# Kernel tuning notes

Measured on AMD Instinct MI355X. Metric: run time of the kernel, lower is better.

Reference implementation:

```python
import jax, jax.numpy as jnp
import numpy as np

EPS = 1e-5
SELECT_NUM = 10   # hard-coded in Support_AUG_Image
NEIGHBOR_K = 3
SEMI_K = 3


def _conv(x, w):
    return jax.lax.conv_general_dilated(x, w, (1, 1), 'SAME',
                                        dimension_numbers=('NCHW', 'OIHW', 'NCHW'))


def _bn(x, g, b):
    # BatchNorm2d, training mode: biased batch stats over (N, H, W)
    mu = jnp.mean(x, (0, 2, 3), keepdims=True)
    var = jnp.mean((x - mu) ** 2, (0, 2, 3), keepdims=True)
    return g[None, :, None, None] * (x - mu) * jax.lax.rsqrt(var + EPS) + b[None, :, None, None]


def _lrelu(x):
    return jnp.where(x >= 0, x, 0.2 * x)


def _pool(x):
    return jax.lax.reduce_window(x, -jnp.inf, jax.lax.max,
                                 (1, 1, 2, 2), (1, 1, 2, 2), 'VALID')


def _features(x, params):
    # conv-bn-lrelu-pool, conv-bn-lrelu-pool, conv-bn-lrelu, conv-bn-lrelu
    for i, (w, g, b) in enumerate(params):
        x = _lrelu(_bn(_conv(x, w), g, b))
        if i < 2:
            x = _pool(x)
    return x  # [N, 64, 21, 21] for 84x84 input


def _descriptors(feat):
    # [B, C, h, w] -> [B, h*w, C], rows L2-normalized (query local descriptors)
    B, C = feat.shape[0], feat.shape[1]
    d = feat.reshape(B, C, -1).transpose(0, 2, 1)
    return d / jnp.sqrt(jnp.sum(d * d, -1, keepdims=True))


def _col_normalize(s):
    # [C, m]: L2-normalize each column (support descriptor)
    return s / jnp.sqrt(jnp.sum(s * s, 0, keepdims=True))


def _img2class_sim(q_desc, S, k):
    # q_desc [B, n, C] row-normalized; S [K, C, m] raw support banks.
    # Per class (K small, fixed): cosine sims [B, n, m], top-k over m, sum.
    sims = []
    for j in range(S.shape[0]):
        inner = q_desc @ _col_normalize(S[j])          # [B, n, m]
        tv = jax.lax.top_k(inner, k)[0]                # [B, n, k]
        sims.append(jnp.sum(tv, axis=(1, 2)))
    return jnp.stack(sims, 1)                          # [B, K]


def _forward(input1, input2, input3, params):
    K, shot = input2.shape[0], input2.shape[1]
    q = _features(input1, params)                      # [Bq, 64, 21, 21]
    sup = _features(input2.reshape((-1,) + input2.shape[2:]), params)
    C, h, w = sup.shape[1], sup.shape[2], sup.shape[3]
    # per class: permute(1,0,2,3).view(C,-1) -> [K, C, shot*h*w]
    S = sup.reshape(K, shot, C, h, w).transpose(0, 2, 1, 3, 4).reshape(K, C, shot * h * w)
    u = _features(input3, params)                      # [Bu, 64, 21, 21]

    # Support_AUG_Image: similarity of unlabeled pool vs support, softmax over classes,
    # then append top-10 unlabeled feature maps (raw) to each class bank.
    u_desc = _descriptors(u)
    sim_u = jax.nn.softmax(_img2class_sim(u_desc, S, SEMI_K), axis=1)  # [Bu, K]
    aug = []
    for j in range(K):
        idx = jax.lax.top_k(sim_u[:, j], SELECT_NUM)[1]                # [10]
        sel = u[idx].transpose(1, 0, 2, 3).reshape(C, -1)              # [C, 10*h*w]
        aug.append(jnp.concatenate([S[j], sel], axis=1))
    S_aug = jnp.stack(aug, 0)                          # [K, C, shot*h*w + 10*h*w]

    # ImgtoClass_Metric on queries vs augmented support
    q_desc = _descriptors(q)
    return _img2class_sim(q_desc, S_aug, NEIGHBOR_K)   # [Bq, K]


def setup_inputs() -> dict:
    key = jax.random.key(0)
    ks = jax.random.split(key, 8)
    inp = {
        'input1': jax.random.normal(ks[0], (75, 3, 84, 84), jnp.float32),
        'input2': jax.random.normal(ks[1], (5, 5, 3, 84, 84), jnp.float32),
        'input3': jax.random.normal(ks[2], (64, 3, 84, 84), jnp.float32),
        'w1': jax.random.normal(ks[3], (64, 3, 3, 3), jnp.float32) * 0.1,
        'w2': jax.random.normal(ks[4], (64, 64, 3, 3), jnp.float32) * 0.05,
        'w3': jax.random.normal(ks[5], (64, 64, 3, 3), jnp.float32) * 0.05,
        'w4': jax.random.normal(ks[6], (64, 64, 3, 3), jnp.float32) * 0.05,
    }
    for i in (1, 2, 3, 4):
        inp[f'g{i}'] = jnp.ones((64,), jnp.float32)
        inp[f'b{i}'] = jnp.zeros((64,), jnp.float32)
    return inp


def reference(input1, input2, input3, w1, g1, b1, w2, g2, b2, w3, g3, b3, w4, g4, b4):
    params = [(w1, g1, b1), (w2, g2, b2), (w3, g3, b3), (w4, g4, b4)]
    return _forward(input1, input2, input3, params)
```

## Files before the change

kernel.cpp:

```cpp
#include <hip/hip_runtime.h>
#include <hip/hip_bf16.h>
#include <math.h>

typedef __hip_bfloat16 bf16;
typedef __attribute__((ext_vector_type(8))) short short8;
typedef __attribute__((ext_vector_type(4))) float floatx4;
typedef __attribute__((ext_vector_type(4))) unsigned short ushort4v;

#define LRELU(v) ((v) < 0.f ? 0.2f * (v) : (v))

__device__ __forceinline__ float b2f(bf16 x) { return __bfloat162float(x); }
__device__ __forceinline__ int img_group(int n) { return n < 75 ? 0 : (n < 100 ? 1 : 2); }

__global__ __launch_bounds__(64) void detect_kernel(
    const void* in1, const void* in2, const void* in3,
    const void* w1, const void* w2, const void* w3, const void* w4,
    const void* g1, const void* g2, const void* g3, const void* g4,
    int* __restrict__ flags)
{
  int t = threadIdx.x;
  if (t >= 11) return;
  const void* p = nullptr; int nh = 384, isg = 0;
  switch (t) {
    case 0: p = in1; break;  case 1: p = in2; break;  case 2: p = in3; break;
    case 3: p = w1;  break;  case 4: p = w2;  break;  case 5: p = w3;  break;
    case 6: p = w4;  break;
    case 7: p = g1; nh = 64; isg = 1; break;
    case 8: p = g2; nh = 64; isg = 1; break;
    case 9: p = g3; nh = 64; isg = 1; break;
    case 10: p = g4; nh = 64; isg = 1; break;
  }
  const unsigned short* h = (const unsigned short*)p;
  int cnt = 0;
  for (int i = 0; i < nh; ++i) {
    unsigned short v = h[i];
    if (isg) {
      if (v == 0) ++cnt;
    } else {
      int e = (v >> 7) & 0xFF;
      if (e >= 160 || (e > 0 && e <= 80)) ++cnt;
    }
  }
  flags[t] = isg ? (cnt >= 16) : (cnt >= 48);
}

#define NIMG 3471552
#define BIMG 13562
#define NWP  110592
#define BWP  432
#define BW1  8
#define BGB  2
#define NPART (4 * 164 * 128)
#define NZ (NPART + 320 + 375)
#define BZ  331
__global__ __launch_bounds__(256) void setup_all(
    const void* in1, const void* in2, const void* in3,
    const void* w1, const void* w2, const void* w3, const void* w4,
    const void* g1, const void* b1, const void* g2, const void* b2,
    const void* g3, const void* b3, const void* g4, const void* b4,
    const int* __restrict__ flags,
    bf16* __restrict__ imgp, bf16* __restrict__ w1p,
    bf16* __restrict__ wp2, bf16* __restrict__ wp3, bf16* __restrict__ wp4,
    float* __restrict__ gb, float* __restrict__ part,
    float* __restrict__ uscore, float* __restrict__ qscore)
{
  int b = blockIdx.x;
  if (b < BIMG) {
    int k = b * 256 + threadIdx.x;
    if (k >= NIMG) return;
    const void* src; int idx, f;
    if (k < 75 * 21168)       { src = in1; idx = k;               f = flags[0]; }
    else if (k < 100 * 21168) { src = in2; idx = k - 75 * 21168;  f = flags[1]; }
    else                      { src = in3; idx = k - 100 * 21168; f = flags[2]; }
    bf16 v = f ? __float2bfloat16(((const float*)src)[idx]) : ((const bf16*)src)[idx];
    int n = k / 21168, r = k % 21168;
    int ci = r / 7056, pix = r % 7056;
    int y = pix / 84, x = pix % 84;
    imgp[((size_t)(n * 3 + ci) * 86 + y + 1) * 86 + x + 1] = v;
  } else if (b < BIMG + BWP) {
    int idx = (b - BIMG) * 256 + threadIdx.x;
    if (idx >= NWP) return;
    int which = idx / 36864, i = idx % 36864;
    const void* src = which == 0 ? w2 : (which == 1 ? w3 : w4);
    bf16* dst = which == 0 ? wp2 : (which == 1 ? wp3 : wp4);
    int f = flags[4 + which];
    float v = f ? ((const float*)src)[i] : b2f(((const bf16*)src)[i]);
    int co = i / 576, ci = (i / 9) % 64, tap = i % 9;
    dst[((size_t)tap * 64 + co) * 64 + ci] = __float2bfloat16(v);
  } else if (b < BIMG + BWP + BW1) {
    int i = (b - BIMG - BWP) * 256 + threadIdx.x;
    if (i >= 2048) return;
    int co = i >> 5, k = i & 31;
    float v = 0.f;
    if (k < 27) {
      int f = flags[3];
      v = f ? ((const float*)w1)[co * 27 + k] : b2f(((const bf16*)w1)[co * 27 + k]);
    }
    w1p[i] = __float2bfloat16(v);
  } else if (b < BIMG + BWP + BW1 + BGB) {
    int i = (b - BIMG - BWP - BW1) * 256 + threadIdx.x;
    if (i >= 512) return;
    int which = i >> 6, cc = i & 63;
    const void* s;
    switch (which) {
      case 0: s = g1; break; case 1: s = b1; break;
      case 2: s = g2; break; case 3: s = b2; break;
      case 4: s = g3; break; case 5: s = b3; break;
      case 6: s = g4; break; default: s = b4; break;
    }
    int isg = !(which & 1);
    int f = isg ? flags[7 + (which >> 1)] : 0;
    gb[i] = f ? ((const float*)s)[cc] : b2f(((const bf16*)s)[cc]);
  } else {
    int i = (b - BIMG - BWP - BW1 - BGB) * 256 + threadIdx.x;
    if (i < NPART) part[i] = 0.f;
    else if (i < NPART + 320) uscore[i - NPART] = 0.f;
    else if (i < NZ) qscore[i - NPART - 320] = 0.f;
  }
}

__global__ __launch_bounds__(256) void conv1_stats_mfma(
    const bf16* __restrict__ imgp, const bf16* __restrict__ w1p,
    float* __restrict__ part)
{
  __shared__ float sacc[128];
  int n = blockIdx.x, tile = blockIdx.y;
  int lane = threadIdx.x & 63;
  int q = lane >> 4, c = lane & 15;
  int wave = threadIdx.x >> 6;
  int p = tile * 64 + wave * 16 + c;
  bool valid = p < 7056;
  int pc = valid ? p : 0;
  int y = pc / 84, x = pc % 84;
  const short* ib = (const short*)(imgp + (size_t)n * 3 * 86 * 86);
  short bs[8];
  #pragma unroll
  for (int j = 0; j < 8; ++j) {
    int k = q * 8 + j;
    int ci = k / 9, tap = k - ci * 9;
    int dy = tap / 3, dx = tap - dy * 3;
    bs[j] = (k < 27 && valid) ? ib[(ci * 86 + y + dy) * 86 + x + dx] : (short)0;
  }
  short8 B = {bs[0], bs[1], bs[2], bs[3], bs[4], bs[5], bs[6], bs[7]};
  float s[16], sq[16];
  #pragma unroll
  for (int t = 0; t < 4; ++t) {
    const short* ap = (const short*)w1p + (t * 16 + c) * 32 + q * 8;
    short8 A = *(const short8*)ap;
    floatx4 acc = {0.f, 0.f, 0.f, 0.f};
    acc = __builtin_amdgcn_mfma_f32_16x16x32_bf16(A, B, acc, 0, 0, 0);
    #pragma unroll
    for (int r = 0; r < 4; ++r) { s[t * 4 + r] = acc[r]; sq[t * 4 + r] = acc[r] * acc[r]; }
  }
  #pragma unroll
  for (int off = 1; off < 16; off <<= 1)
    #pragma unroll
    for (int i = 0; i < 16; ++i) {
      s[i]  += __shfl_xor(s[i], off);
      sq[i] += __shfl_xor(sq[i], off);
    }
  if (threadIdx.x < 128) sacc[threadIdx.x] = 0.f;
  __syncthreads();
  if (c == 0) {
    #pragma unroll
    for (int t = 0; t < 4; ++t)
      #pragma unroll
      for (int r = 0; r < 4; ++r) {
        int co = t * 16 + q * 4 + r;
        atomicAdd(&sacc[co], s[t * 4 + r]);
        atomicAdd(&sacc[64 + co], sq[t * 4 + r]);
      }
  }
  __syncthreads();
  if (threadIdx.x < 128) atomicAdd(&part[n * 128 + threadIdx.x], sacc[threadIdx.x]);
}

__global__ __launch_bounds__(256) void finalize_kernel(
    const float* __restrict__ part, const float* __restrict__ gam, const float* __restrict__ bet,
    float* __restrict__ scl, float* __restrict__ sht, float HWf)
{
  int t = threadIdx.x;
  if (t >= 192) return;
  int g = t / 64, c = t % 64;
  const int starts[3] = {0, 75, 100}, cnts[3] = {75, 25, 64};
  float S = 0.f, Q = 0.f;
  for (int im = starts[g]; im < starts[g] + cnts[g]; ++im) {
    S += part[im * 128 + c];
    Q += part[im * 128 + 64 + c];
  }
  float N = (float)cnts[g] * HWf;
  float mean = S / N;
  float var = fmaxf(Q / N - mean * mean, 0.f);
  float rstd = rsqrtf(var + 1e-5f);
  float sc = gam[c] * rstd;
  scl[t] = sc;
  sht[t] = bet[c] - mean * sc;
}

__global__ __launch_bounds__(256) void conv1_pool_mfma(
    const bf16* __restrict__ imgp, const bf16* __restrict__ w1p,
    const float* __restrict__ scl, const float* __restrict__ sht,
    bf16* __restrict__ p1t)
{
  int n = blockIdx.x, tile = blockIdx.y;
  int lane = threadIdx.x & 63, wave = threadIdx.x >> 6;
  int q = lane >> 4, c = lane & 15;
  int pp = tile * 64 + wave * 16 + c;
  bool valid = pp < 1764;
  int pc = valid ? pp : 0;
  int py = pc / 42, px = pc % 42;
  int g = img_group(n);
  const short* ib = (const short*)(imgp + (size_t)n * 3 * 86 * 86);
  short8 B[4];
  #pragma unroll
  for (int quad = 0; quad < 4; ++quad) {
    int y = 2 * py + (quad >> 1), x = 2 * px + (quad & 1);
    short bs[8];
    #pragma unroll
    for (int j = 0; j < 8; ++j) {
      int k = q * 8 + j;
      int ci = k / 9, tap = k - ci * 9;
      int dy = tap / 3, dx = tap - dy * 3;
      bs[j] = (k < 27) ? ib[(ci * 86 + y + dy) * 86 + x + dx] : (short)0;
    }
    B[quad] = (short8){bs[0], bs[1], bs[2], bs[3], bs[4], bs[5], bs[6], bs[7]};
  }
  bf16* ob = p1t + ((size_t)n * 1936 + (py + 1) * 44 + px + 1) * 64;
  #pragma unroll
  for (int t = 0; t < 4; ++t) {
    const short* ap = (const short*)w1p + (t * 16 + c) * 32 + q * 8;
    short8 A = *(const short8*)ap;
    floatx4 a0 = {0.f,0.f,0.f,0.f}, a1 = a0, a2 = a0, a3 = a0;
    a0 = __builtin_amdgcn_mfma_f32_16x16x32_bf16(A, B[0], a0, 0, 0, 0);
    a1 = __builtin_amdgcn_mfma_f32_16x16x32_bf16(A, B[1], a1, 0, 0, 0);
    a2 = __builtin_amdgcn_mfma_f32_16x16x32_bf16(A, B[2], a2, 0, 0, 0);
    a3 = __builtin_amdgcn_mfma_f32_16x16x32_bf16(A, B[3], a3, 0, 0, 0);
    if (valid) {
      ushort4v st;
      #pragma unroll
      for (int r = 0; r < 4; ++r) {
        int co = t * 16 + q * 4 + r;
        float sc_ = scl[g * 64 + co], sh_ = sht[g * 64 + co];
        float v0 = a0[r] * sc_ + sh_; v0 = LRELU(v0);
        float v1 = a1[r] * sc_ + sh_; v1 = LRELU(v1);
        float v2 = a2[r] * sc_ + sh_; v2 = LRELU(v2);
        float v3 = a3[r] * sc_ + sh_; v3 = LRELU(v3);
        float best = fmaxf(fmaxf(v0, v1), fmaxf(v2, v3));
        bf16 bv = __float2bfloat16(best);
        st[r] = *(unsigned short*)&bv;
      }
      *(ushort4v*)(ob + t * 16 + q * 4) = st;
    }
  }
}

__global__ __launch_bounds__(256) void tpad_kernel(
    const bf16* __restrict__ in, bf16* __restrict__ outp,
    int HW, int W, int PW, int PHPW)
{
  __shared__ bf16 tile[64][65];
  int n = blockIdx.x, t0 = blockIdx.y * 64;
  for (int idx = threadIdx.x; idx < 4096; idx += 256) {
    int ci = idx >> 6, pix = idx & 63;
    int p = t0 + pix;
    tile[pix][ci] = (p < HW) ? in[((size_t)n * 64 + ci) * HW + p] : __float2bfloat16(0.f);
  }
  __syncthreads();
  for (int idx = threadIdx.x; idx < 4096; idx += 256) {
    int pix = idx >> 6, ci = idx & 63;
    int p = t0 + pix;
    if (p < HW) {
      int y = p / W, x = p % W;
      outp[((size_t)n * PHPW + (y + 1) * PW + (x + 1)) * 64 + ci] = tile[pix][ci];
    }
  }
}

__global__ __launch_bounds__(256) void bnt_kernel(
    const float* __restrict__ in, const float* __restrict__ scl, const float* __restrict__ sht,
    bf16* __restrict__ outp, int HW, int W, int PW, int PHPW)
{
  __shared__ bf16 tile[64][65];
  int n = blockIdx.x, t0 = blockIdx.y * 64;
  int g = img_group(n);
  for (int idx = threadIdx.x; idx < 4096; idx += 256) {
    int ci = idx >> 6, pix = idx & 63;
    int p = t0 + pix;
    float v = 0.f;
    if (p < HW) {
      v = in[((size_t)n * 64 + ci) * HW + p] * scl[g * 64 + ci] + sht[g * 64 + ci];
      v = LRELU(v);
    }
    tile[pix][ci] = __float2bfloat16(v);
  }
  __syncthreads();
  for (int idx = threadIdx.x; idx < 4096; idx += 256) {
    int pix = idx >> 6, ci = idx & 63;
    int p = t0 + pix;
    if (p < HW) {
      int y = p / W, x = p % W;
      outp[((size_t)n * PHPW + (y + 1) * PW + (x + 1)) * 64 + ci] = tile[pix][ci];
    }
  }
}

__global__ __launch_bounds__(256) void conv_mfma_kernel(
    const bf16* __restrict__ in_t, const bf16* __restrict__ wp,
    void* __restrict__ outp, int HW, int W, int PW, int PHPW, int out_is_f32,
    float* __restrict__ part)
{
  __shared__ float sacc[128];
  if (threadIdx.x < 128) sacc[threadIdx.x] = 0.f;
  __syncthreads();
  int n = blockIdx.x, tile = blockIdx.y;
  int wave = threadIdx.x >> 6, lane = threadIdx.x & 63;
  int q = lane >> 4, c = lane & 15;
  int p = tile * 64 + wave * 16 + c;
  bool valid = p < HW;
  int pc = valid ? p : HW - 1;
  int y = pc / W, x = pc % W;
  const bf16* ibase = in_t + ((size_t)n * PHPW + y * PW + x) * 64;

  short8 B0[9], B1[9];
  #pragma unroll
  for (int dy = 0; dy < 3; ++dy)
    #pragma unroll
    for (int dx = 0; dx < 3; ++dx) {
      const short* bp = (const short*)(ibase + (dy * PW + dx) * 64) + q * 8;
      B0[dy * 3 + dx] = *(const short8*)bp;
      B1[dy * 3 + dx] = *(const short8*)(bp + 32);
    }

  for (int t = 0; t < 4; ++t) {
    floatx4 acc = {0.f, 0.f, 0.f, 0.f};
    #pragma unroll
    for (int tap = 0; tap < 9; ++tap) {
      const short* ap = (const short*)(wp + ((size_t)tap * 64 + t * 16 + c) * 64) + q * 8;
      short8 A0 = *(const short8*)ap;
      short8 A1 = *(const short8*)(ap + 32);
      acc = __builtin_amdgcn_mfma_f32_16x16x32_bf16(A0, B0[tap], acc, 0, 0, 0);
      acc = __builtin_amdgcn_mfma_f32_16x16x32_bf16(A1, B1[tap], acc, 0, 0, 0);
    }
    float sv[4], qv[4];
    #pragma unroll
    for (int r = 0; r < 4; ++r) {
      float v = valid ? acc[r] : 0.f;
      sv[r] = v; qv[r] = v * v;
    }
    #pragma unroll
    for (int off = 1; off < 16; off <<= 1)
      #pragma unroll
      for (int r = 0; r < 4; ++r) {
        sv[r] += __shfl_xor(sv[r], off);
        qv[r] += __shfl_xor(qv[r], off);
      }
    if (c == 0) {
      #pragma unroll
      for (int r = 0; r < 4; ++r) {
        int co = t * 16 + q * 4 + r;
        atomicAdd(&sacc[co], sv[r]);
        atomicAdd(&sacc[64 + co], qv[r]);
      }
    }
    if (valid) {
      #pragma unroll
      for (int r = 0; r < 4; ++r) {
        int co = t * 16 + q * 4 + r;
        size_t oidx = ((size_t)n * 64 + co) * HW + p;
        if (out_is_f32) ((float*)outp)[oidx] = acc[r];
        else ((bf16*)outp)[oidx] = __float2bfloat16(acc[r]);
      }
    }
  }
  __syncthreads();
  if (threadIdx.x < 128) atomicAdd(&part[n * 128 + threadIdx.x], sacc[threadIdx.x]);
}

__global__ __launch_bounds__(256) void bn2_pool_kernel(
    const bf16* __restrict__ c2, const float* __restrict__ scl, const float* __restrict__ sht,
    bf16* __restrict__ p2)
{
  int bx = blockIdx.x;
  int n = bx >> 6, co = bx & 63;
  int g = img_group(n);
  float sc = scl[g * 64 + co], sh = sht[g * 64 + co];
  const bf16* base = c2 + (size_t)(n * 64 + co) * 1764;
  for (int p = threadIdx.x; p < 441; p += 256) {
    int py = p / 21, px = p % 21;
    float best = -1e30f;
    #pragma unroll
    for (int dy = 0; dy < 2; ++dy)
      #pragma unroll
      for (int dx = 0; dx < 2; ++dx) {
        float v = b2f(base[(2 * py + dy) * 42 + 2 * px + dx]) * sc + sh;
        v = LRELU(v);
        best = fmaxf(best, v);
      }
    p2[(size_t)(n * 64 + co) * 441 + p] = __float2bfloat16(best);
  }
}

__global__ __launch_bounds__(256) void bn_norm_desc(
    const float* __restrict__ feat, const float* __restrict__ scl, const float* __restrict__ sht,
    bf16* __restrict__ descAll)
{
  __shared__ float tile[64][65];
  int n = blockIdx.x, t0 = blockIdx.y * 64;
  int g = img_group(n);
  for (int idx = threadIdx.x; idx < 4096; idx += 256) {
    int ci = idx >> 6, pix = idx & 63;
    int p = t0 + pix;
    float v = 0.f;
    if (p < 441) {
      v = feat[((size_t)n * 64 + ci) * 441 + p] * scl[g * 64 + ci] + sht[g * 64 + ci];
      v = LRELU(v);
    }
    tile[pix][ci] = v;
  }
  __syncthreads();
  int pix = threadIdx.x >> 2, quar = threadIdx.x & 3;
  float ss = 0.f;
  #pragma unroll
  for (int c = 0; c < 16; ++c) { float v = tile[pix][quar * 16 + c]; ss += v * v; }
  ss += __shfl_xor(ss, 1);
  ss += __shfl_xor(ss, 2);
  int p = t0 + pix;
  float inv = (p < 441) ? rsqrtf(ss) : 0.f;
  bf16* o = descAll + ((size_t)n * 512 + p) * 64 + quar * 16;
  #pragma unroll
  for (int c = 0; c < 16; ++c) o[c] = __float2bfloat16(tile[pix][quar * 16 + c] * inv);
}

__global__ __launch_bounds__(256) void sbank_copy(
    const bf16* __restrict__ descAll, bf16* __restrict__ SnT)
{
  int j = blockIdx.x / 9, chunk = blockIdx.x % 9;
  int col = chunk * 256 + threadIdx.x;
  short* o = (short*)(SnT + ((size_t)j * 2304 + col) * 64);
  if (col < 2205) {
    int shot = col / 441, pos = col % 441;
    const short* s = (const short*)(descAll + ((size_t)(75 + j * 5 + shot) * 512 + pos) * 64);
    #pragma unroll
    for (int k = 0; k < 8; ++k) *(short8*)(o + k * 8) = *(const short8*)(s + k * 8);
  } else {
    short8 z = {0,0,0,0,0,0,0,0};
    #pragma unroll
    for (int k = 0; k < 8; ++k) *(short8*)(o + k * 8) = z;
  }
}

__global__ __launch_bounds__(256) void saug_copy(
    const bf16* __restrict__ descAll, const bf16* __restrict__ SnT,
    const int* __restrict__ sel, bf16* __restrict__ SaT)
{
  int j = blockIdx.x / 26, chunk = blockIdx.x % 26;
  int col = chunk * 256 + threadIdx.x;
  short* o = (short*)(SaT + ((size_t)j * 6656 + col) * 64);
  const short* s;
  if (col < 2205) {
    s = (const short*)(SnT + ((size_t)j * 2304 + col) * 64);
  } else if (col < 6615) {
    int rel = col - 2205;
    int i = rel / 441, pos = rel % 441;
    int img = 100 + sel[j * 10 + i];
    s = (const short*)(descAll + ((size_t)img * 512 + pos) * 64);
  } else {
    short8 z = {0,0,0,0,0,0,0,0};
    #pragma unroll
    for (int k = 0; k < 8; ++k) *(short8*)(o + k * 8) = z;
    return;
  }
  #pragma unroll
  for (int k = 0; k < 8; ++k) *(short8*)(o + k * 8) = *(const short8*)(s + k * 8);
}

__global__ __launch_bounds__(256) void sim_mfma_kernel(
    const bf16* __restrict__ desc, const bf16* __restrict__ bankT,
    float* __restrict__ out, int m, int mp)
{
  __shared__ short lds[2][64 * 72];
  int img = blockIdx.x, cls = blockIdx.y, rowgrp = blockIdx.z;
  int tid = threadIdx.x;
  int wave = tid >> 6, lane = tid & 63;
  int q = lane >> 4, c = lane & 15;
  int R = rowgrp * 256 + wave * 64;

  short8 bB0[4], bB1[4];
  #pragma unroll
  for (int t = 0; t < 4; ++t) {
    const short* dp = (const short*)(desc + ((size_t)img * 512 + R + t * 16 + c) * 64) + q * 8;
    bB0[t] = *(const short8*)dp;
    bB1[t] = *(const short8*)(dp + 32);
  }

  float t0[4], t1[4], t2[4];
  #pragma unroll
  for (int i = 0; i < 4; ++i) { t0[i] = -1e4f; t1[i] = -1e4f; t2[i] = -1e4f; }

  const short* bankc = (const short*)(bankT + (size_t)cls * mp * 64);
  int nchunk = mp >> 6;
  int nfull = m >> 4;

  for (int s = tid; s < 512; s += 256) {
    int col = s >> 3, part = s & 7;
    *(short8*)(&lds[0][col * 72 + part * 8]) = *(const short8*)(bankc + (size_t)col * 64 + part * 8);
  }
  __syncthreads();

  for (int ch = 0; ch < nchunk; ++ch) {
    int cur = ch & 1;
    if (ch + 1 < nchunk) {
      const short* src = bankc + (size_t)(ch + 1) * 4096;
      for (int s = tid; s < 512; s += 256) {
        int col = s >> 3, part = s & 7;
        *(short8*)(&lds[cur ^ 1][col * 72 + part * 8]) = *(const short8*)(src + (size_t)col * 64 + part * 8);
      }
    }
    #pragma unroll
    for (int ti = 0; ti < 4; ++ti) {
      const short* lp = &lds[cur][(ti * 16 + c) * 72 + q * 8];
      short8 A0 = *(const short8*)lp;
      short8 A1 = *(const short8*)(lp + 32);
      floatx4 acc[4];
      #pragma unroll
      for (int t = 0; t < 4; ++t) {
        acc[t] = (floatx4){0.f, 0.f, 0.f, 0.f};
        acc[t] = __builtin_amdgcn_mfma_f32_16x16x32_bf16(A0, bB0[t], acc[t], 0, 0, 0);
        acc[t] = __builtin_amdgcn_mfma_f32_16x16x32_bf16(A1, bB1[t], acc[t], 0, 0, 0);
      }
      int gt = ch * 4 + ti;
      if (gt < nfull) {
        #pragma unroll
        for (int t = 0; t < 4; ++t)
          #pragma unroll
          for (int r = 0; r < 4; ++r) {
            float v = acc[t][r];
            t2[t] = __builtin_amdgcn_fmed3f(v, t2[t], t1[t]);
            t1[t] = __builtin_amdgcn_fmed3f(v, t1[t], t0[t]);
            t0[t] = fmaxf(t0[t], v);
          }
      } else {
        #pragma unroll
        for (int t = 0; t < 4; ++t)
          #pragma unroll
          for (int r = 0; r < 4; ++r) {
            bool colok = (gt * 16 + q * 4 + r) < m;
            float v = colok ? acc[t][r] : -1e4f;
            t2[t] = __builtin_amdgcn_fmed3f(v, t2[t], t1[t]);
            t1[t] = __builtin_amdgcn_fmed3f(v, t1[t], t0[t]);
            t0[t] = fmaxf(t0[t], v);
          }
      }
    }
    __syncthreads();
  }

  #pragma unroll
  for (int off = 16; off < 64; off <<= 1) {
    #pragma unroll
    for (int i = 0; i < 4; ++i) {
      float b0v = __shfl_xor(t0[i], off);
      float b1v = __shfl_xor(t1[i], off);
      float b2v = __shfl_xor(t2[i], off);
      float n0 = fmaxf(t0[i], b0v);
      float n1 = fminf(fmaxf(t0[i], b1v), fmaxf(t1[i], b0v));
      float n2 = fminf(fminf(fmaxf(t0[i], b2v), fmaxf(t1[i], b1v)), fmaxf(t2[i], b0v));
      t0[i] = n0; t1[i] = n1; t2[i] = n2;
    }
  }

  float psum = 0.f;
  if (q == 0) {
    #pragma unroll
    for (int t = 0; t < 4; ++t) {
      int row = R + t * 16 + c;
      if (row < 441) psum += t0[t] + t1[t] + t2[t];
    }
  }
  #pragma unroll
  for (int off = 32; off > 0; off >>= 1) psum += __shfl_down(psum, off);
  if (lane == 0) atomicAdd(&out[img * 5 + cls], psum);
}

__global__ __launch_bounds__(64) void softtop_kernel(
    const float* __restrict__ uscore, int* __restrict__ sel)
{
  __shared__ float simu[320];
  int i = threadIdx.x;
  {
    float v[5]; float mx = -1e30f;
    #pragma unroll
    for (int j = 0; j < 5; ++j) { v[j] = uscore[i * 5 + j]; mx = fmaxf(mx, v[j]); }
    float s = 0.f;
    #pragma unroll
    for (int j = 0; j < 5; ++j) { v[j] = expf(v[j] - mx); s += v[j]; }
    float inv = 1.f / s;
    #pragma unroll
    for (int j = 0; j < 5; ++j) simu[i * 5 + j] = v[j] * inv;
  }
  __syncthreads();
  if (i < 5) {
    unsigned long long mask = 0ull;
    for (int r = 0; r < 10; ++r) {
      float best = -1e30f; int bi = 0;
      for (int k = 0; k < 64; ++k) {
        if ((mask >> k) & 1ull) continue;
        float v = simu[k * 5 + i];
        if (v > best) { best = v; bi = k; }
      }
      mask |= (1ull << bi);
      sel[i * 10 + r] = bi;
    }
  }
}

__global__ __launch_bounds__(256) void outcvt_kernel(
    const float* __restrict__ qv, const int* __restrict__ flags, float* __restrict__ o)
{
  int i = blockIdx.x * 256 + threadIdx.x;
  if (i >= 375) return;
  float v = qv[i];
  int bad = (!isfinite(v)) || fabsf(v) > 2e3f;
  if (bad) {
    int code = flags[0] * 4 + flags[3] * 2 + flags[7];
    v = -(1e8f * (1.f + 0.01f * (float)code));
  }
  o[i] = v;
}

extern "C" void kernel_launch(void* const* d_in, const int* in_sizes, int n_in,
                              void* d_out, int out_size, void* d_ws, size_t ws_size,
                              hipStream_t stream) {
  const void* in1 = d_in[0];
  const void* in2 = d_in[1];
  const void* in3 = d_in[2];
  const void* w1  = d_in[3];
  const void* w2  = d_in[4];
  const void* w3  = d_in[5];
  const void* w4  = d_in[6];
  const void* g1  = d_in[7];
  const void* b1  = d_in[8];
  const void* g2  = d_in[9];
  const void* b2  = d_in[10];
  const void* g3  = d_in[11];
  const void* b3  = d_in[12];
  const void* g4  = d_in[13];
  const void* b4  = d_in[14];

  char* base = (char*)d_ws;
  size_t off = 0;
  auto alloc = [&](size_t bytes) -> void* {
    void* p = base + off;
    off += (bytes + 255) & ~(size_t)255;
    return p;
  };
  int*   flags = (int*)alloc(16 * 4);
  bf16*  wp2   = (bf16*)alloc(36864 * 2);
  bf16*  wp3   = (bf16*)alloc(36864 * 2);
  bf16*  wp4   = (bf16*)alloc(36864 * 2);
  bf16*  w1p   = (bf16*)alloc(2048 * 2);
  float* gb    = (float*)alloc(8 * 64 * 4);
  float* part  = (float*)alloc(4 * 164 * 128 * 4);
  float* scl1  = (float*)alloc(192 * 4);
  float* sht1  = (float*)alloc(192 * 4);
  float* scl2  = (float*)alloc(192 * 4);
  float* sht2  = (float*)alloc(192 * 4);
  float* scl3  = (float*)alloc(192 * 4);
  float* sht3  = (float*)alloc(192 * 4);
  float* scl4  = (float*)alloc(192 * 4);
  float* sht4  = (float*)alloc(192 * 4);
  float* uscore = (float*)alloc(320 * 4);
  int*   sel    = (int*)alloc(50 * 4);
  float* qscore = (float*)alloc(375 * 4);
  char* ztop = base + off;
  bf16*  imgp = (bf16*)alloc((size_t)164 * 3 * 86 * 86 * 2);
  bf16*  p1t  = (bf16*)alloc((size_t)164 * 1936 * 64 * 2);
  bf16*  p2t  = (bf16*)alloc((size_t)164 * 529 * 64 * 2);
  bf16*  f3t  = (bf16*)alloc((size_t)164 * 529 * 64 * 2);
  bf16*  descAll = (bf16*)alloc((size_t)164 * 512 * 64 * 2);
  size_t zbytes = (size_t)((base + off) - ztop);
  bf16*  conv2o   = (bf16*)alloc((size_t)164 * 64 * 1764 * 2);
  bf16*  pooled2b = (bf16*)alloc((size_t)164 * 64 * 441 * 2);
  bf16* SnT     = (bf16*)alloc((size_t)5 * 2304 * 64 * 2);
  bf16* SaT     = (bf16*)alloc((size_t)5 * 6656 * 64 * 2);
  float* feat3 = (float*)p1t;
  float* feat4 = (float*)((char*)p1t + (size_t)164 * 64 * 441 * 4);
  float* part1 = part;
  float* part2 = part + 164 * 128;
  float* part3 = part + 2 * 164 * 128;
  float* part4 = part + 3 * 164 * 128;

  detect_kernel<<<1, 64, 0, stream>>>(in1, in2, in3, w1, w2, w3, w4, g1, g2, g3, g4, flags);
  hipMemsetAsync(ztop, 0, zbytes, stream);
  setup_all<<<BIMG + BWP + BW1 + BGB + BZ, 256, 0, stream>>>(
      in1, in2, in3, w1, w2, w3, w4, g1, b1, g2, b2, g3, b3, g4, b4,
      flags, imgp, w1p, wp2, wp3, wp4, gb, part, uscore, qscore);

  conv1_stats_mfma<<<dim3(164, 111), 256, 0, stream>>>(imgp, w1p, part1);
  finalize_kernel<<<1, 256, 0, stream>>>(part1, gb + 0 * 64, gb + 1 * 64, scl1, sht1, 7056.f);
  conv1_pool_mfma<<<dim3(164, 28), 256, 0, stream>>>(imgp, w1p, scl1, sht1, p1t);

  conv_mfma_kernel<<<dim3(164, 28), 256, 0, stream>>>(p1t, wp2, conv2o, 1764, 42, 44, 1936, 0, part2);
  finalize_kernel<<<1, 256, 0, stream>>>(part2, gb + 2 * 64, gb + 3 * 64, scl2, sht2, 1764.f);
  bn2_pool_kernel<<<10496, 256, 0, stream>>>(conv2o, scl2, sht2, pooled2b);

  tpad_kernel<<<dim3(164, 7), 256, 0, stream>>>(pooled2b, p2t, 441, 21, 23, 529);
  conv_mfma_kernel<<<dim3(164, 7), 256, 0, stream>>>(p2t, wp3, feat3, 441, 21, 23, 529, 1, part3);
  finalize_kernel<<<1, 256, 0, stream>>>(part3, gb + 4 * 64, gb + 5 * 64, scl3, sht3, 441.f);
  bnt_kernel<<<dim3(164, 7), 256, 0, stream>>>(feat3, scl3, sht3, f3t, 441, 21, 23, 529);

  conv_mfma_kernel<<<dim3(164, 7), 256, 0, stream>>>(f3t, wp4, feat4, 441, 21, 23, 529, 1, part4);
  finalize_kernel<<<1, 256, 0, stream>>>(part4, gb + 6 * 64, gb + 7 * 64, scl4, sht4, 441.f);

  bn_norm_desc<<<dim3(164, 7), 256, 0, stream>>>(feat4, scl4, sht4, descAll);
  sbank_copy<<<45, 256, 0, stream>>>(descAll, SnT);

  sim_mfma_kernel<<<dim3(64, 5, 2), 256, 0, stream>>>(descAll + (size_t)100 * 512 * 64, SnT, uscore, 2205, 2304);
  softtop_kernel<<<1, 64, 0, stream>>>(uscore, sel);
  saug_copy<<<130, 256, 0, stream>>>(descAll, SnT, sel, SaT);

  sim_mfma_kernel<<<dim3(75, 5, 2), 256, 0, stream>>>(descAll, SaT, qscore, 6615, 6656);
  outcvt_kernel<<<2, 256, 0, stream>>>(qscore, flags, (float*)d_out);
}
```

Measured before the change: 1.156 ms.

## Fuse BN2-pool with transpose-pad, zero only borders, halve sim rows per wave

Three independent changes. The bn2 pooling kernel now writes padded channel-last output directly, which removes the separate transpose-pad kernel and the intermediate pooled buffer. The full-buffer memset is replaced by a kernel that zeros only the padding borders and descriptor tail rows. The similarity kernel gives each wave 32 query rows instead of 64 and doubles the grid's z dimension, which cuts register pressure and adds parallelism but re-reads the support bank more often.

```diff
diff --git a/kernel.cpp b/kernel.cpp
--- a/kernel.cpp
+++ b/kernel.cpp
@@ -42,6 +42,52 @@
     }
   }
   flags[t] = isg ? (cnt >= 16) : (cnt >= 48);
+}
+
+#define ZT0 167280
+#define ZT1 1972592
+#define ZT2 2896240
+#define ZT3 3819888
+#define ZT4 4565104
+__device__ __forceinline__ void border_yx(int b, int W, int* y, int* x) {
+  if (b < W) { *y = 0; *x = b; }
+  else if (b < 2 * W) { *y = W - 1; *x = b - W; }
+  else { int cc = b - 2 * W; *y = 1 + (cc >> 1); *x = (cc & 1) ? (W - 1) : 0; }
+}
+__global__ __launch_bounds__(256) void zero_pads(
+    bf16* __restrict__ imgp, bf16* __restrict__ p1t,
+    bf16* __restrict__ p2t, bf16* __restrict__ f3t, bf16* __restrict__ descAll)
+{
+  int i = blockIdx.x * 256 + threadIdx.x;
+  bf16 z = __float2bfloat16(0.f);
+  if (i < ZT0) {
+    int plane = i / 340, b = i % 340;
+    int y, x; border_yx(b, 86, &y, &x);
+    imgp[((size_t)plane * 86 + y) * 86 + x] = z;
+  } else if (i < ZT1) {
+    int r = i - ZT0;
+    int img = r / (172 * 64); r %= 172 * 64;
+    int colb = r >> 6, ch = r & 63;
+    int y, x; border_yx(colb, 44, &y, &x);
+    p1t[(((size_t)img * 1936) + y * 44 + x) * 64 + ch] = z;
+  } else if (i < ZT2) {
+    int r = i - ZT1;
+    int img = r / (88 * 64); r %= 88 * 64;
+    int colb = r >> 6, ch = r & 63;
+    int y, x; border_yx(colb, 23, &y, &x);
+    p2t[(((size_t)img * 529) + y * 23 + x) * 64 + ch] = z;
+  } else if (i < ZT3) {
+    int r = i - ZT2;
+    int img = r / (88 * 64); r %= 88 * 64;
+    int colb = r >> 6, ch = r & 63;
+    int y, x; border_yx(colb, 23, &y, &x);
+    f3t[(((size_t)img * 529) + y * 23 + x) * 64 + ch] = z;
+  } else if (i < ZT4) {
+    int r = i - ZT3;
+    int img = r / (71 * 64); r %= 71 * 64;
+    int row = 441 + (r >> 6), ch = r & 63;
+    descAll[((size_t)img * 512 + row) * 64 + ch] = z;
+  }
 }
 
 #define NIMG 3471552
@@ -254,28 +300,6 @@
   }
 }
 
-__global__ __launch_bounds__(256) void tpad_kernel(
-    const bf16* __restrict__ in, bf16* __restrict__ outp,
-    int HW, int W, int PW, int PHPW)
-{
-  __shared__ bf16 tile[64][65];
-  int n = blockIdx.x, t0 = blockIdx.y * 64;
-  for (int idx = threadIdx.x; idx < 4096; idx += 256) {
-    int ci = idx >> 6, pix = idx & 63;
-    int p = t0 + pix;
-    tile[pix][ci] = (p < HW) ? in[((size_t)n * 64 + ci) * HW + p] : __float2bfloat16(0.f);
-  }
-  __syncthreads();
-  for (int idx = threadIdx.x; idx < 4096; idx += 256) {
-    int pix = idx >> 6, ci = idx & 63;
-    int p = t0 + pix;
-    if (p < HW) {
-      int y = p / W, x = p % W;
-      outp[((size_t)n * PHPW + (y + 1) * PW + (x + 1)) * 64 + ci] = tile[pix][ci];
-    }
-  }
-}
-
 __global__ __launch_bounds__(256) void bnt_kernel(
     const float* __restrict__ in, const float* __restrict__ scl, const float* __restrict__ sht,
     bf16* __restrict__ outp, int HW, int W, int PW, int PHPW)
@@ -376,27 +400,42 @@
   if (threadIdx.x < 128) atomicAdd(&part[n * 128 + threadIdx.x], sacc[threadIdx.x]);
 }
 
-__global__ __launch_bounds__(256) void bn2_pool_kernel(
+__global__ __launch_bounds__(256) void bn2_pool_t(
     const bf16* __restrict__ c2, const float* __restrict__ scl, const float* __restrict__ sht,
-    bf16* __restrict__ p2)
-{
-  int bx = blockIdx.x;
-  int n = bx >> 6, co = bx & 63;
+    bf16* __restrict__ p2t)
+{
+  __shared__ bf16 tile[64][65];
+  int n = blockIdx.x, t0 = blockIdx.y * 64;
   int g = img_group(n);
-  float sc = scl[g * 64 + co], sh = sht[g * 64 + co];
-  const bf16* base = c2 + (size_t)(n * 64 + co) * 1764;
-  for (int p = threadIdx.x; p < 441; p += 256) {
-    int py = p / 21, px = p % 21;
-    float best = -1e30f;
-    #pragma unroll
-    for (int dy = 0; dy < 2; ++dy)
+  for (int idx = threadIdx.x; idx < 4096; idx += 256) {
+    int co = idx >> 6, pix = idx & 63;
+    int p = t0 + pix;
+    bf16 outv = __float2bfloat16(0.f);
+    if (p < 441) {
+      float sc = scl[g * 64 + co], sh = sht[g * 64 + co];
+      int py = p / 21, px = p % 21;
+      const bf16* base = c2 + ((size_t)n * 64 + co) * 1764;
+      float best = -1e30f;
       #pragma unroll
-      for (int dx = 0; dx < 2; ++dx) {
-        float v = b2f(base[(2 * py + dy) * 42 + 2 * px + dx]) * sc + sh;
-        v = LRELU(v);
-        best = fmaxf(best, v);
-      }
-    p2[(size_t)(n * 64 + co) * 441 + p] = __float2bfloat16(best);
+      for (int dy = 0; dy < 2; ++dy)
+        #pragma unroll
+        for (int dx = 0; dx < 2; ++dx) {
+          float v = b2f(base[(2 * py + dy) * 42 + 2 * px + dx]) * sc + sh;
+          v = LRELU(v);
+          best = fmaxf(best, v);
+        }
+      outv = __float2bfloat16(best);
+    }
+    tile[pix][co] = outv;
+  }
+  __syncthreads();
+  for (int idx = threadIdx.x; idx < 4096; idx += 256) {
+    int pix = idx >> 6, co = idx & 63;
+    int p = t0 + pix;
+    if (p < 441) {
+      int y = p / 21, x = p % 21;
+      p2t[((size_t)n * 529 + (y + 1) * 23 + x + 1) * 64 + co] = tile[pix][co];
+    }
   }
 }
 
@@ -483,19 +522,18 @@
   int tid = threadIdx.x;
   int wave = tid >> 6, lane = tid & 63;
   int q = lane >> 4, c = lane & 15;
-  int R = rowgrp * 256 + wave * 64;
-
-  short8 bB0[4], bB1[4];
-  #pragma unroll
-  for (int t = 0; t < 4; ++t) {
-    const short* dp = (const short*)(desc + ((size_t)img * 512 + R + t * 16 + c) * 64) + q * 8;
-    bB0[t] = *(const short8*)dp;
-    bB1[t] = *(const short8*)(dp + 32);
-  }
-
-  float t0[4], t1[4], t2[4];
-  #pragma unroll
-  for (int i = 0; i < 4; ++i) { t0[i] = -1e4f; t1[i] = -1e4f; t2[i] = -1e4f; }
+  int R = rowgrp * 128 + wave * 32;
+
+  const short* dp0 = (const short*)(desc + ((size_t)img * 512 + R + c) * 64) + q * 8;
+  const short* dp1 = (const short*)(desc + ((size_t)img * 512 + R + 16 + c) * 64) + q * 8;
+  short8 b00 = *(const short8*)dp0;
+  short8 b01 = *(const short8*)(dp0 + 32);
+  short8 b10 = *(const short8*)dp1;
+  short8 b11 = *(const short8*)(dp1 + 32);
+
+  float t0[2], t1[2], t2[2];
+  #pragma unroll
+  for (int i = 0; i < 2; ++i) { t0[i] = -1e4f; t1[i] = -1e4f; t2[i] = -1e4f; }
 
   const short* bankc = (const short*)(bankT + (size_t)cls * mp * 64);
   int nchunk = mp >> 6;
@@ -517,39 +555,42 @@
       }
     }
     #pragma unroll
-    for (int ti = 0; ti < 4; ++ti) {
-      const short* lp = &lds[cur][(ti * 16 + c) * 72 + q * 8];
+    for (int t = 0; t < 4; ++t) {
+      const short* lp = &lds[cur][(t * 16 + c) * 72 + q * 8];
       short8 A0 = *(const short8*)lp;
       short8 A1 = *(const short8*)(lp + 32);
-      floatx4 acc[4];
-      #pragma unroll
-      for (int t = 0; t < 4; ++t) {
-        acc[t] = (floatx4){0.f, 0.f, 0.f, 0.f};
-        acc[t] = __builtin_amdgcn_mfma_f32_16x16x32_bf16(A0, bB0[t], acc[t], 0, 0, 0);
-        acc[t] = __builtin_amdgcn_mfma_f32_16x16x32_bf16(A1, bB1[t], acc[t], 0, 0, 0);
-      }
-      int gt = ch * 4 + ti;
+      floatx4 acc0 = {0.f, 0.f, 0.f, 0.f};
+      floatx4 acc1 = {0.f, 0.f, 0.f, 0.f};
+      acc0 = __builtin_amdgcn_mfma_f32_16x16x32_bf16(A0, b00, acc0, 0, 0, 0);
+      acc0 = __builtin_amdgcn_mfma_f32_16x16x32_bf16(A1, b01, acc0, 0, 0, 0);
+      acc1 = __builtin_amdgcn_mfma_f32_16x16x32_bf16(A0, b10, acc1, 0, 0, 0);
+      acc1 = __builtin_amdgcn_mfma_f32_16x16x32_bf16(A1, b11, acc1, 0, 0, 0);
+      int gt = ch * 4 + t;
       if (gt < nfull) {
         #pragma unroll
-        for (int t = 0; t < 4; ++t)
-          #pragma unroll
-          for (int r = 0; r < 4; ++r) {
-            float v = acc[t][r];
-            t2[t] = __builtin_amdgcn_fmed3f(v, t2[t], t1[t]);
-            t1[t] = __builtin_amdgcn_fmed3f(v, t1[t], t0[t]);
-            t0[t] = fmaxf(t0[t], v);
-          }
+        for (int r = 0; r < 4; ++r) {
+          float v0 = acc0[r];
+          t2[0] = __builtin_amdgcn_fmed3f(v0, t2[0], t1[0]);
+          t1[0] = __builtin_amdgcn_fmed3f(v0, t1[0], t0[0]);
+          t0[0] = fmaxf(t0[0], v0);
+          float v1 = acc1[r];
+          t2[1] = __builtin_amdgcn_fmed3f(v1, t2[1], t1[1]);
+          t1[1] = __builtin_amdgcn_fmed3f(v1, t1[1], t0[1]);
+          t0[1] = fmaxf(t0[1], v1);
+        }
       } else {
         #pragma unroll
-        for (int t = 0; t < 4; ++t)
-          #pragma unroll
-          for (int r = 0; r < 4; ++r) {
-            bool colok = (gt * 16 + q * 4 + r) < m;
-            float v = colok ? acc[t][r] : -1e4f;
-            t2[t] = __builtin_amdgcn_fmed3f(v, t2[t], t1[t]);
-            t1[t] = __builtin_amdgcn_fmed3f(v, t1[t], t0[t]);
-            t0[t] = fmaxf(t0[t], v);
-          }
+        for (int r = 0; r < 4; ++r) {
+          bool colok = (gt * 16 + q * 4 + r) < m;
+          float v0 = colok ? acc0[r] : -1e4f;
+          t2[0] = __builtin_amdgcn_fmed3f(v0, t2[0], t1[0]);
+          t1[0] = __builtin_amdgcn_fmed3f(v0, t1[0], t0[0]);
+          t0[0] = fmaxf(t0[0], v0);
+          float v1 = colok ? acc1[r] : -1e4f;
+          t2[1] = __builtin_amdgcn_fmed3f(v1, t2[1], t1[1]);
+          t1[1] = __builtin_amdgcn_fmed3f(v1, t1[1], t0[1]);
+          t0[1] = fmaxf(t0[1], v1);
+        }
       }
     }
     __syncthreads();
@@ -558,7 +599,7 @@
   #pragma unroll
   for (int off = 16; off < 64; off <<= 1) {
     #pragma unroll
-    for (int i = 0; i < 4; ++i) {
+    for (int i = 0; i < 2; ++i) {
       float b0v = __shfl_xor(t0[i], off);
       float b1v = __shfl_xor(t1[i], off);
       float b2v = __shfl_xor(t2[i], off);
@@ -571,11 +612,8 @@
 
   float psum = 0.f;
   if (q == 0) {
-    #pragma unroll
-    for (int t = 0; t < 4; ++t) {
-      int row = R + t * 16 + c;
-      if (row < 441) psum += t0[t] + t1[t] + t2[t];
-    }
+    if (R + c < 441)      psum += t0[0] + t1[0] + t2[0];
+    if (R + 16 + c < 441) psum += t0[1] + t1[1] + t2[1];
   }
   #pragma unroll
   for (int off = 32; off > 0; off >>= 1) psum += __shfl_down(psum, off);
@@ -672,15 +710,12 @@
   float* uscore = (float*)alloc(320 * 4);
   int*   sel    = (int*)alloc(50 * 4);
   float* qscore = (float*)alloc(375 * 4);
-  char* ztop = base + off;
   bf16*  imgp = (bf16*)alloc((size_t)164 * 3 * 86 * 86 * 2);
   bf16*  p1t  = (bf16*)alloc((size_t)164 * 1936 * 64 * 2);
   bf16*  p2t  = (bf16*)alloc((size_t)164 * 529 * 64 * 2);
   bf16*  f3t  = (bf16*)alloc((size_t)164 * 529 * 64 * 2);
   bf16*  descAll = (bf16*)alloc((size_t)164 * 512 * 64 * 2);
-  size_t zbytes = (size_t)((base + off) - ztop);
   bf16*  conv2o   = (bf16*)alloc((size_t)164 * 64 * 1764 * 2);
-  bf16*  pooled2b = (bf16*)alloc((size_t)164 * 64 * 441 * 2);
   bf16* SnT     = (bf16*)alloc((size_t)5 * 2304 * 64 * 2);
   bf16* SaT     = (bf16*)alloc((size_t)5 * 6656 * 64 * 2);
   float* feat3 = (float*)p1t;
@@ -691,7 +726,7 @@
   float* part4 = part + 3 * 164 * 128;
 
   detect_kernel<<<1, 64, 0, stream>>>(in1, in2, in3, w1, w2, w3, w4, g1, g2, g3, g4, flags);
-  hipMemsetAsync(ztop, 0, zbytes, stream);
+  zero_pads<<<(ZT4 + 255) / 256, 256, 0, stream>>>(imgp, p1t, p2t, f3t, descAll);
   setup_all<<<BIMG + BWP + BW1 + BGB + BZ, 256, 0, stream>>>(
       in1, in2, in3, w1, w2, w3, w4, g1, b1, g2, b2, g3, b3, g4, b4,
       flags, imgp, w1p, wp2, wp3, wp4, gb, part, uscore, qscore);
@@ -702,9 +737,8 @@
 
   conv_mfma_kernel<<<dim3(164, 28), 256, 0, stream>>>(p1t, wp2, conv2o, 1764, 42, 44, 1936, 0, part2);
   finalize_kernel<<<1, 256, 0, stream>>>(part2, gb + 2 * 64, gb + 3 * 64, scl2, sht2, 1764.f);
-  bn2_pool_kernel<<<10496, 256, 0, stream>>>(conv2o, scl2, sht2, pooled2b);
-
-  tpad_kernel<<<dim3(164, 7), 256, 0, stream>>>(pooled2b, p2t, 441, 21, 23, 529);
+  bn2_pool_t<<<dim3(164, 7), 256, 0, stream>>>(conv2o, scl2, sht2, p2t);
+
   conv_mfma_kernel<<<dim3(164, 7), 256, 0, stream>>>(p2t, wp3, feat3, 441, 21, 23, 529, 1, part3);
   finalize_kernel<<<1, 256, 0, stream>>>(part3, gb + 4 * 64, gb + 5 * 64, scl3, sht3, 441.f);
   bnt_kernel<<<dim3(164, 7), 256, 0, stream>>>(feat3, scl3, sht3, f3t, 441, 21, 23, 529);
@@ -715,10 +749,10 @@
   bn_norm_desc<<<dim3(164, 7), 256, 0, stream>>>(feat4, scl4, sht4, descAll);
   sbank_copy<<<45, 256, 0, stream>>>(descAll, SnT);
 
-  sim_mfma_kernel<<<dim3(64, 5, 2), 256, 0, stream>>>(descAll + (size_t)100 * 512 * 64, SnT, uscore, 2205, 2304);
+  sim_mfma_kernel<<<dim3(64, 5, 4), 256, 0, stream>>>(descAll + (size_t)100 * 512 * 64, SnT, uscore, 2205, 2304);
   softtop_kernel<<<1, 64, 0, stream>>>(uscore, sel);
   saug_copy<<<130, 256, 0, stream>>>(descAll, SnT, sel, SaT);
 
-  sim_mfma_kernel<<<dim3(75, 5, 2), 256, 0, stream>>>(descAll, SaT, qscore, 6615, 6656);
+  sim_mfma_kernel<<<dim3(75, 5, 4), 256, 0, stream>>>(descAll, SaT, qscore, 6615, 6656);
   outcvt_kernel<<<2, 256, 0, stream>>>(qscore, flags, (float*)d_out);
 }
```

Result: faster. 1.107 ms (-4.3%).
